# Performance work log

Hardware: AMD Instinct MI355X
Metric: run time of the kernel (lower is better)

Reference implementation:

```python
import jax, jax.numpy as jnp
import numpy as np
import math

B, S, DM = 2, 2048, 2048
NH, NKV, HD = 16, 4, 128
DFF = 8192
K_KEEP = DFF // 2  # sparsity_ratio = 0.5
EPS = 1e-6


def setup_inputs() -> dict:
    key = jax.random.key(0)
    ks = jax.random.split(key, 10)
    sc = 0.02
    return {
        "hidden_states": jax.random.normal(ks[0], (B, S, DM), dtype=jnp.float32),
        "wq": jax.random.normal(ks[1], (NH * HD, DM), dtype=jnp.float32) * sc,
        "wk": jax.random.normal(ks[2], (NKV * HD, DM), dtype=jnp.float32) * sc,
        "wv": jax.random.normal(ks[3], (NKV * HD, DM), dtype=jnp.float32) * sc,
        "wo": jax.random.normal(ks[4], (DM, NH * HD), dtype=jnp.float32) * sc,
        "ln1_w": jnp.ones((DM,), dtype=jnp.float32),
        "ln2_w": jnp.ones((DM,), dtype=jnp.float32),
        "w_gate": jax.random.normal(ks[5], (DFF, DM), dtype=jnp.float32) * sc,
        "w_up": jax.random.normal(ks[6], (DFF, DM), dtype=jnp.float32) * sc,
        "w_down": jax.random.normal(ks[7], (DM, DFF), dtype=jnp.float32) * sc,
    }


def _rmsnorm(x, w):
    var = jnp.mean(x * x, axis=-1, keepdims=True)
    return x * jax.lax.rsqrt(var + EPS) * w


def reference(hidden_states, wq, wk, wv, wo, ln1_w, ln2_w, w_gate, w_up, w_down):
    b, s, _ = hidden_states.shape
    # --- attention sub-block: RMSNorm -> GQA causal attention -> residual ---
    x = _rmsnorm(hidden_states, ln1_w)
    q = (x @ wq.T).reshape(b, s, NH, HD)
    k = (x @ wk.T).reshape(b, s, NKV, HD)
    v = (x @ wv.T).reshape(b, s, NKV, HD)
    # expand KV heads to match query heads (GQA)
    rep = NH // NKV
    k = jnp.repeat(k, rep, axis=2)
    v = jnp.repeat(v, rep, axis=2)
    scores = jnp.einsum('bqhd,bkhd->bhqk', q, k) / math.sqrt(HD)
    causal = jnp.tril(jnp.ones((s, s), dtype=bool))
    scores = jnp.where(causal, scores, jnp.finfo(scores.dtype).min)
    attn = jax.nn.softmax(scores, axis=-1)
    o = jnp.einsum('bhqk,bkhd->bqhd', attn, v).reshape(b, s, NH * HD)
    h = hidden_states + o @ wo.T
    # --- FFN sub-block: RMSNorm -> TopK-sparse SwiGLU -> residual ---
    y = _rmsnorm(h, ln2_w)
    gate = jax.nn.silu(y @ w_gate.T)  # [b, s, DFF]
    mag = jnp.abs(gate)
    thr = jax.lax.top_k(mag, K_KEEP)[0][..., -1:]  # kth-largest magnitude
    gate = jnp.where(mag >= thr, gate, 0.0)
    ff = (gate * (y @ w_up.T)) @ w_down.T
    return h + ff
```

## Files before the change

### kernel.cpp

```cpp
#include <hip/hip_runtime.h>
#include <stdint.h>

constexpr int SEQ    = 2048;
constexpr int DMODEL = 2048;
constexpr int NHEADS = 16;
constexpr int NKVH   = 4;
constexpr int HDIM   = 128;
constexpr int DFFN   = 8192;
constexpr int BATCH  = 2;
constexpr int MTOK   = BATCH * SEQ;
constexpr int KKEEP  = DFFN / 2;

typedef __bf16 bf16x8 __attribute__((ext_vector_type(8)));
typedef float  f32x4  __attribute__((ext_vector_type(4)));
typedef unsigned short u16;
typedef unsigned int   u32;

__device__ __forceinline__ u16 f2bu(float f) {
  u32 x = __builtin_bit_cast(u32, f);
  return (u16)((x + 0x7FFFu + ((x >> 16) & 1u)) >> 16);
}
__device__ __forceinline__ float b2f(u16 u) {
  u32 v = ((u32)u) << 16;
  return __builtin_bit_cast(float, v);
}
__device__ __forceinline__ void gl_lds16(const void* g, void* l) {
  __builtin_amdgcn_global_load_lds((const __attribute__((address_space(1))) u32*)g,
                                   (__attribute__((address_space(3))) u32*)l, 16, 0, 0);
}

__global__ __launch_bounds__(256) void cvt_kernel(const float* __restrict__ in,
                                                  u16* __restrict__ out, int n) {
  int i = (blockIdx.x * 256 + threadIdx.x) * 4;
  if (i >= n) return;
  float4 v = *(const float4*)(in + i);
  uint2 pk;
  pk.x = (u32)f2bu(v.x) | ((u32)f2bu(v.y) << 16);
  pk.y = (u32)f2bu(v.z) | ((u32)f2bu(v.w) << 16);
  *(uint2*)(out + i) = pk;
}

__global__ __launch_bounds__(256) void rmsnorm_kernel(const float* __restrict__ in,
                                                      const float* __restrict__ w,
                                                      u16* __restrict__ out) {
  const int tid = threadIdx.x;
  const size_t row = blockIdx.x;
  const float* x = in + row * DMODEL;
  float4 v0 = *(const float4*)(x + tid * 4);
  float4 v1 = *(const float4*)(x + 1024 + tid * 4);
  float s = v0.x*v0.x + v0.y*v0.y + v0.z*v0.z + v0.w*v0.w
          + v1.x*v1.x + v1.y*v1.y + v1.z*v1.z + v1.w*v1.w;
#pragma unroll
  for (int off = 1; off < 64; off <<= 1) s += __shfl_xor(s, off, 64);
  __shared__ float wsum[4];
  if ((tid & 63) == 0) wsum[tid >> 6] = s;
  __syncthreads();
  s = wsum[0] + wsum[1] + wsum[2] + wsum[3];
  const float rinv = rsqrtf(s * (1.0f / DMODEL) + 1e-6f);
  u16* o = out + row * DMODEL;
#pragma unroll
  for (int part = 0; part < 2; ++part) {
    int c = part * 1024 + tid * 4;
    float4 vv = (part == 0) ? v0 : v1;
    float4 wv = *(const float4*)(w + c);
    uint2 pk;
    pk.x = (u32)f2bu(vv.x * rinv * wv.x) | ((u32)f2bu(vv.y * rinv * wv.y) << 16);
    pk.y = (u32)f2bu(vv.z * rinv * wv.z) | ((u32)f2bu(vv.w * rinv * wv.w) << 16);
    *(uint2*)(o + c) = pk;
  }
}

template <int EPI>
__global__ __launch_bounds__(256, 2)
void gemm_bt(const u16* __restrict__ A, const u16* __restrict__ B,
             void* __restrict__ C, const float* res,
             int M, int N, int K) {
  __shared__ u16 As[128 * 64];
  __shared__ u16 Bs[128 * 64];
  const int tid = threadIdx.x;
  const int wave = tid >> 6, lane = tid & 63;
  const int m0 = blockIdx.y * 128, n0 = blockIdx.x * 128;
  const int r_in = lane >> 3, chk = lane & 7;
  const int fk = lane >> 4, fc = lane & 15;
  const int wm = (wave >> 1) * 64, wn = (wave & 1) * 64;
  f32x4 acc[4][4] = {};

  for (int kt = 0; kt < K; kt += 64) {
    __syncthreads();
#pragma unroll
    for (int i = 0; i < 4; ++i) {
      int row = wave * 32 + i * 8 + r_in;
      int gc = chk ^ (row & 7);
      gl_lds16(A + (size_t)(m0 + row) * K + kt + gc * 8, As + (wave * 32 + i * 8) * 64);
    }
#pragma unroll
    for (int i = 0; i < 4; ++i) {
      int row = wave * 32 + i * 8 + r_in;
      int gc = chk ^ (row & 7);
      gl_lds16(B + (size_t)(n0 + row) * K + kt + gc * 8, Bs + (wave * 32 + i * 8) * 64);
    }
    __syncthreads();
#pragma unroll
    for (int kk = 0; kk < 2; ++kk) {
      bf16x8 a[4], b[4];
#pragma unroll
      for (int i = 0; i < 4; ++i) {
        int row = wm + i * 16 + fc;
        int c = (kk * 4 + fk) ^ (row & 7);
        a[i] = *(const bf16x8*)(As + row * 64 + c * 8);
      }
#pragma unroll
      for (int j = 0; j < 4; ++j) {
        int row = wn + j * 16 + fc;
        int c = (kk * 4 + fk) ^ (row & 7);
        b[j] = *(const bf16x8*)(Bs + row * 64 + c * 8);
      }
#pragma unroll
      for (int i = 0; i < 4; ++i)
#pragma unroll
        for (int j = 0; j < 4; ++j)
          acc[i][j] = __builtin_amdgcn_mfma_f32_16x16x32_bf16(a[i], b[j], acc[i][j], 0, 0, 0);
    }
  }

  const int rb = fk * 4;
#pragma unroll
  for (int i = 0; i < 4; ++i) {
#pragma unroll
    for (int j = 0; j < 4; ++j) {
      int row = m0 + wm + i * 16 + rb;
      int col = n0 + wn + j * 16 + fc;
      f32x4 v = acc[i][j];
      if constexpr (EPI == 0) {
        u16* o = (u16*)C;
#pragma unroll
        for (int r = 0; r < 4; ++r) o[(size_t)(row + r) * N + col] = f2bu(v[r]);
      } else if constexpr (EPI == 1) {
        u16* o = (u16*)C;
        int bb = row >> 11, s = row & (SEQ - 1);
        int kvh = col >> 7, d = col & (HDIM - 1);
        size_t base = (((size_t)bb * NKVH + kvh) * HDIM + d) * SEQ + s;
        uint2 pk;
        pk.x = (u32)f2bu(v[0]) | ((u32)f2bu(v[1]) << 16);
        pk.y = (u32)f2bu(v[2]) | ((u32)f2bu(v[3]) << 16);
        *(uint2*)(o + base) = pk;
      } else if constexpr (EPI == 2) {
        float* o = (float*)C;
#pragma unroll
        for (int r = 0; r < 4; ++r) {
          size_t idx = (size_t)(row + r) * N + col;
          float rv = res[idx];
          o[idx] = v[r] + rv;
        }
      } else {
        float* o = (float*)C;
#pragma unroll
        for (int r = 0; r < 4; ++r) {
          float g = v[r];
          o[(size_t)(row + r) * N + col] = g / (1.0f + __expf(-g));
        }
      }
    }
  }
}

__global__ __launch_bounds__(256, 2)
void attn_kernel(const u16* __restrict__ Q, const u16* __restrict__ Kb,
                 const u16* __restrict__ Vt, u16* __restrict__ O) {
  __shared__ u16 Ks[32 * 128];
  __shared__ u16 Vs[128 * 32];
  __shared__ u16 Ps[4][16 * 32];
  const int tid = threadIdx.x, wave = tid >> 6, lane = tid & 63;
  const int qt = blockIdx.x, h = blockIdx.y, b = blockIdx.z;
  const int kvh = h >> 2;
  const int q0 = qt * 64, qw = q0 + wave * 16;
  const int fk = lane >> 4, fc = lane & 15;
  const float SC = 0.08838834764831845f;

  bf16x8 qf[4];
  {
    const u16* qp = Q + ((size_t)(b * SEQ + qw + fc)) * DMODEL + h * HDIM + fk * 8;
#pragma unroll
    for (int f = 0; f < 4; ++f) qf[f] = *(const bf16x8*)(qp + f * 32);
  }
  f32x4 oacc[8] = {};
  float m_run[4] = {-1e30f, -1e30f, -1e30f, -1e30f};
  float l_run[4] = {0.f, 0.f, 0.f, 0.f};
  const int nt = (q0 + 64) / 32;
  const int kr = lane >> 4, kc = lane & 15;
  const int vr = lane >> 2, vc = lane & 3;

  for (int t = 0; t < nt; ++t) {
    const int k0 = t * 32;
    __syncthreads();
#pragma unroll
    for (int ii = 0; ii < 2; ++ii) {
      int issue = wave * 2 + ii;
      {
        int row = issue * 4 + kr;
        int gc = kc ^ (row & 7);
        gl_lds16(Kb + ((size_t)(b * SEQ + k0 + row)) * (NKVH * HDIM) + kvh * HDIM + gc * 8,
                 Ks + issue * 4 * 128);
      }
      {
        int row = issue * 16 + vr;
        int gc = vc ^ ((row >> 1) & 3);
        gl_lds16(Vt + (((size_t)b * NKVH + kvh) * HDIM + row) * SEQ + k0 + gc * 8,
                 Vs + issue * 16 * 32);
      }
    }
    __syncthreads();
    if (k0 <= qw + 15) {
      f32x4 sf[2] = {};
#pragma unroll
      for (int sb = 0; sb < 2; ++sb) {
#pragma unroll
        for (int f = 0; f < 4; ++f) {
          int kvr = sb * 16 + fc;
          int c = (f * 4 + fk) ^ (kvr & 7);
          bf16x8 kf = *(const bf16x8*)(Ks + kvr * 128 + c * 8);
          sf[sb] = __builtin_amdgcn_mfma_f32_16x16x32_bf16(qf[f], kf, sf[sb], 0, 0, 0);
        }
      }
#pragma unroll
      for (int r = 0; r < 4; ++r) {
        const int qrow = qw + fk * 4 + r;
        float s0 = sf[0][r] * SC, s1 = sf[1][r] * SC;
        if (k0 + fc > qrow) s0 = -1e30f;
        if (k0 + 16 + fc > qrow) s1 = -1e30f;
        float mx = fmaxf(s0, s1);
#pragma unroll
        for (int off = 1; off < 16; off <<= 1) mx = fmaxf(mx, __shfl_xor(mx, off, 64));
        float mnew = fmaxf(m_run[r], mx);
        float p0 = __expf(s0 - mnew), p1 = __expf(s1 - mnew);
        float rs = p0 + p1;
#pragma unroll
        for (int off = 1; off < 16; off <<= 1) rs += __shfl_xor(rs, off, 64);
        float alpha = __expf(m_run[r] - mnew);
        m_run[r] = mnew;
        l_run[r] = l_run[r] * alpha + rs;
#pragma unroll
        for (int f = 0; f < 8; ++f) oacc[f][r] *= alpha;
        const int prow = fk * 4 + r;
        const int key = (prow >> 1) & 3;
        Ps[wave][prow * 32 + ((((fc >> 3)) ^ key) << 3) + (fc & 7)] = f2bu(p0);
        Ps[wave][prow * 32 + ((((fc >> 3) + 2) ^ key) << 3) + (fc & 7)] = f2bu(p1);
      }
      bf16x8 pf = *(const bf16x8*)(&Ps[wave][fc * 32 + ((fk ^ ((fc >> 1) & 3)) << 3)]);
#pragma unroll
      for (int f = 0; f < 8; ++f) {
        int d = f * 16 + fc;
        int c = fk ^ ((d >> 1) & 3);
        bf16x8 vf = *(const bf16x8*)(Vs + d * 32 + c * 8);
        oacc[f] = __builtin_amdgcn_mfma_f32_16x16x32_bf16(pf, vf, oacc[f], 0, 0, 0);
      }
    }
  }
  u16* op = O + ((size_t)(b * SEQ + qw + fk * 4)) * DMODEL + h * HDIM + fc;
#pragma unroll
  for (int r = 0; r < 4; ++r) {
    float inv = 1.0f / l_run[r];
#pragma unroll
    for (int f = 0; f < 8; ++f) op[(size_t)r * DMODEL + f * 16] = f2bu(oacc[f][r] * inv);
  }
}

__global__ __launch_bounds__(256)
void topk_kernel(const float* __restrict__ gate, u16* __restrict__ upact) {
  __shared__ u32 sabs[DFFN];
  __shared__ u32 hist[4][256];
  __shared__ u32 ss[257];
  __shared__ u32 sh_prefix, sh_rem;
  const int tid = threadIdx.x, wave = tid >> 6;
  const size_t row = blockIdx.x;
  const float* g = gate + row * DFFN;
  for (int it = 0; it < 4; ++it) {
    int e = it * 2048 + tid * 8;
    float4 a = *(const float4*)(g + e);
    float4 b = *(const float4*)(g + e + 4);
    sabs[e + 0] = __builtin_bit_cast(u32, a.x);
    sabs[e + 1] = __builtin_bit_cast(u32, a.y);
    sabs[e + 2] = __builtin_bit_cast(u32, a.z);
    sabs[e + 3] = __builtin_bit_cast(u32, a.w);
    sabs[e + 4] = __builtin_bit_cast(u32, b.x);
    sabs[e + 5] = __builtin_bit_cast(u32, b.y);
    sabs[e + 6] = __builtin_bit_cast(u32, b.z);
    sabs[e + 7] = __builtin_bit_cast(u32, b.w);
  }
  if (tid == 0) { sh_prefix = 0; sh_rem = KKEEP; }
  __syncthreads();
  for (int pass = 0; pass < 4; ++pass) {
    const int p = 24 - pass * 8;
    const u32 mask_hi = (pass == 0) ? 0u : (0xFFFFFFFFu << (p + 8));
    for (int i = tid; i < 1024; i += 256) ((u32*)hist)[i] = 0;
    __syncthreads();
    const u32 prefix = sh_prefix, rem = sh_rem;
    for (int it = 0; it < 4; ++it) {
      int e = it * 2048 + tid * 8;
#pragma unroll
      for (int j = 0; j < 8; ++j) {
        u32 mg = sabs[e + j] & 0x7FFFFFFFu;
        if ((mg & mask_hi) == (prefix & mask_hi))
          atomicAdd(&hist[wave][(mg >> p) & 0xFF], 1u);
      }
    }
    __syncthreads();
    ss[tid] = hist[0][tid] + hist[1][tid] + hist[2][tid] + hist[3][tid];
    if (tid == 0) ss[256] = 0;
    __syncthreads();
    for (int off = 1; off < 256; off <<= 1) {
      u32 v = (tid + off < 256) ? ss[tid + off] : 0u;
      __syncthreads();
      ss[tid] += v;
      __syncthreads();
    }
    if (ss[tid] >= rem && ss[tid + 1] < rem) {
      sh_prefix = prefix | ((u32)tid << p);
      sh_rem = rem - ss[tid + 1];
    }
    __syncthreads();
  }
  const u32 thr = sh_prefix;
  u16* ua = upact + row * DFFN;
  for (int it = 0; it < 4; ++it) {
    int e = it * 2048 + tid * 8;
    uint4 uv = *(const uint4*)(ua + e);
    const u16* up16 = (const u16*)&uv;
    u16 outp[8];
#pragma unroll
    for (int j = 0; j < 8; ++j) {
      u32 bits = sabs[e + j];
      u32 mg = bits & 0x7FFFFFFFu;
      float gg = __builtin_bit_cast(float, bits);
      float prod = (mg >= thr) ? gg * b2f(up16[j]) : 0.0f;
      outp[j] = f2bu(prod);
    }
    uint4 ov;
    ov.x = (u32)outp[0] | ((u32)outp[1] << 16);
    ov.y = (u32)outp[2] | ((u32)outp[3] << 16);
    ov.z = (u32)outp[4] | ((u32)outp[5] << 16);
    ov.w = (u32)outp[6] | ((u32)outp[7] << 16);
    *(uint4*)(ua + e) = ov;
  }
}

extern "C" void kernel_launch(void* const* d_in, const int* in_sizes, int n_in,
                              void* d_out, int out_size, void* d_ws, size_t ws_size,
                              hipStream_t stream) {
  const float* hidden = (const float*)d_in[0];
  const float* wq = (const float*)d_in[1];
  const float* wk = (const float*)d_in[2];
  const float* wv = (const float*)d_in[3];
  const float* wo = (const float*)d_in[4];
  const float* ln1 = (const float*)d_in[5];
  const float* ln2 = (const float*)d_in[6];
  const float* wg = (const float*)d_in[7];
  const float* wu = (const float*)d_in[8];
  const float* wd = (const float*)d_in[9];
  float* out = (float*)d_out;
  (void)in_sizes; (void)n_in; (void)out_size;

  size_t off = 0;
  auto alloc = [&](size_t n) { char* r = (char*)d_ws + off; off += (n + 255) & ~(size_t)255; return r; };
  u16* wq_b = (u16*)alloc((size_t)DMODEL * DMODEL * 2);
  u16* wk_b = (u16*)alloc((size_t)NKVH * HDIM * DMODEL * 2);
  u16* wv_b = (u16*)alloc((size_t)NKVH * HDIM * DMODEL * 2);
  u16* wo_b = (u16*)alloc((size_t)DMODEL * DMODEL * 2);
  u16* wg_b = (u16*)alloc((size_t)DFFN * DMODEL * 2);
  u16* tok  = (u16*)alloc((size_t)MTOK * DMODEL * 2);
  u16* upb  = (u16*)alloc((size_t)MTOK * DFFN * 2);
  char* S   = alloc((size_t)(MTOK / 2) * DFFN * 4);
  u16* qb   = (u16*)S;
  u16* kb   = (u16*)(S + (size_t)MTOK * DMODEL * 2);
  u16* vtb  = (u16*)(S + (size_t)MTOK * DMODEL * 2 + (size_t)MTOK * NKVH * HDIM * 2);
  u16* wu_b = (u16*)(S + (size_t)MTOK * DMODEL * 2 + 2 * (size_t)MTOK * NKVH * HDIM * 2);
  float* gateh = (float*)S;
  u16* wd_b = (u16*)S;
  const size_t needed = off;
  if (ws_size < needed) return;

  auto cvt = [&](const float* src, u16* dst, size_t n) {
    cvt_kernel<<<dim3((unsigned)(n / 1024)), 256, 0, stream>>>(src, dst, (int)n);
  };
  cvt(wq, wq_b, (size_t)DMODEL * DMODEL);
  cvt(wk, wk_b, (size_t)NKVH * HDIM * DMODEL);
  cvt(wv, wv_b, (size_t)NKVH * HDIM * DMODEL);
  cvt(wo, wo_b, (size_t)DMODEL * DMODEL);
  cvt(wg, wg_b, (size_t)DFFN * DMODEL);
  cvt(wu, wu_b, (size_t)DFFN * DMODEL);

  rmsnorm_kernel<<<MTOK, 256, 0, stream>>>(hidden, ln1, tok);

  gemm_bt<0><<<dim3(DMODEL / 128, MTOK / 128), 256, 0, stream>>>(
      tok, wq_b, qb, nullptr, MTOK, DMODEL, DMODEL);
  gemm_bt<0><<<dim3(NKVH * HDIM / 128, MTOK / 128), 256, 0, stream>>>(
      tok, wk_b, kb, nullptr, MTOK, NKVH * HDIM, DMODEL);
  gemm_bt<1><<<dim3(NKVH * HDIM / 128, MTOK / 128), 256, 0, stream>>>(
      tok, wv_b, vtb, nullptr, MTOK, NKVH * HDIM, DMODEL);

  attn_kernel<<<dim3(SEQ / 64, NHEADS, BATCH), 256, 0, stream>>>(qb, kb, vtb, tok);

  gemm_bt<2><<<dim3(DMODEL / 128, MTOK / 128), 256, 0, stream>>>(
      tok, wo_b, out, hidden, MTOK, DMODEL, DMODEL);

  rmsnorm_kernel<<<MTOK, 256, 0, stream>>>(out, ln2, tok);

  gemm_bt<0><<<dim3(DFFN / 128, MTOK / 128), 256, 0, stream>>>(
      tok, wu_b, upb, nullptr, MTOK, DFFN, DMODEL);

  for (int half = 0; half < 2; ++half) {
    const u16* yh = tok + (size_t)half * (MTOK / 2) * DMODEL;
    u16* uph = upb + (size_t)half * (MTOK / 2) * DFFN;
    gemm_bt<3><<<dim3(DFFN / 128, (MTOK / 2) / 128), 256, 0, stream>>>(
        yh, wg_b, gateh, nullptr, MTOK / 2, DFFN, DMODEL);
    topk_kernel<<<MTOK / 2, 256, 0, stream>>>(gateh, uph);
  }

  cvt(wd, wd_b, (size_t)DMODEL * DFFN);

  gemm_bt<2><<<dim3(DMODEL / 128, MTOK / 128), 256, 0, stream>>>(
      upb, wd_b, out, out, MTOK, DMODEL, DFFN);
}
```

Baseline: 1.133 ms.

## Rewrite attention with 32x32 MFMA, double-buffered KV, lazy rescale; swizzle GEMM blocks

The attention kernel now uses 128-query blocks with 32 query rows per wave and 32x32x16 MFMAs. It double-buffers the K/V tiles in LDS to overlap loads with compute, and keeps P in registers through lane shuffles instead of staging it in LDS. The softmax skips rescaling unless the running max grows by more than a threshold. The GEMM and attention grids also remap block indices, XCD-style, to improve cache locality. The risks are higher register pressure and fewer attention blocks, which causes more causal load imbalance per block.

```diff
diff --git a/kernel.cpp b/kernel.cpp
--- a/kernel.cpp
+++ b/kernel.cpp
@@ -13,6 +13,7 @@
 
 typedef __bf16 bf16x8 __attribute__((ext_vector_type(8)));
 typedef float  f32x4  __attribute__((ext_vector_type(4)));
+typedef float  f32x16 __attribute__((ext_vector_type(16)));
 typedef unsigned short u16;
 typedef unsigned int   u32;
 
@@ -79,7 +80,10 @@
   __shared__ u16 Bs[128 * 64];
   const int tid = threadIdx.x;
   const int wave = tid >> 6, lane = tid & 63;
-  const int m0 = blockIdx.y * 128, n0 = blockIdx.x * 128;
+  const int nwg = gridDim.x * gridDim.y;
+  const int lin = blockIdx.y * gridDim.x + blockIdx.x;
+  const int swz = (lin & 7) * (nwg >> 3) + (lin >> 3);
+  const int m0 = (swz / gridDim.x) * 128, n0 = (swz % gridDim.x) * 128;
   const int r_in = lane >> 3, chk = lane & 7;
   const int fk = lane >> 4, fc = lane & 15;
   const int wm = (wave >> 1) * 64, wn = (wave & 1) * 64;
@@ -167,101 +171,142 @@
 __global__ __launch_bounds__(256, 2)
 void attn_kernel(const u16* __restrict__ Q, const u16* __restrict__ Kb,
                  const u16* __restrict__ Vt, u16* __restrict__ O) {
-  __shared__ u16 Ks[32 * 128];
-  __shared__ u16 Vs[128 * 32];
-  __shared__ u16 Ps[4][16 * 32];
+  __shared__ u16 Ksh[2 * 32 * 128];
+  __shared__ u16 Vsh[2 * 128 * 32];
   const int tid = threadIdx.x, wave = tid >> 6, lane = tid & 63;
-  const int qt = blockIdx.x, h = blockIdx.y, b = blockIdx.z;
+  const int half = lane >> 5, l31 = lane & 31;
+  const int d_lin = blockIdx.x + gridDim.x * (blockIdx.y + gridDim.y * blockIdx.z);
+  const int lin = (d_lin & 7) * 64 + (d_lin >> 3);
+  const int bx = lin & 15, h = (lin >> 4) & 15, b = lin >> 8;
   const int kvh = h >> 2;
-  const int q0 = qt * 64, qw = q0 + wave * 16;
-  const int fk = lane >> 4, fc = lane & 15;
+  const int qw = bx * 128 + wave * 32;
   const float SC = 0.08838834764831845f;
-
-  bf16x8 qf[4];
+  const int ntb = bx * 4 + 4;
+  const int nmy = bx * 4 + wave;
+
+  bf16x8 qf[8];
   {
-    const u16* qp = Q + ((size_t)(b * SEQ + qw + fc)) * DMODEL + h * HDIM + fk * 8;
-#pragma unroll
-    for (int f = 0; f < 4; ++f) qf[f] = *(const bf16x8*)(qp + f * 32);
-  }
-  f32x4 oacc[8] = {};
-  float m_run[4] = {-1e30f, -1e30f, -1e30f, -1e30f};
-  float l_run[4] = {0.f, 0.f, 0.f, 0.f};
-  const int nt = (q0 + 64) / 32;
-  const int kr = lane >> 4, kc = lane & 15;
-  const int vr = lane >> 2, vc = lane & 3;
-
-  for (int t = 0; t < nt; ++t) {
-    const int k0 = t * 32;
-    __syncthreads();
+    const u16* qp = Q + ((size_t)(b * SEQ + qw + l31)) * DMODEL + h * HDIM + half * 8;
+#pragma unroll
+    for (int s = 0; s < 8; ++s) qf[s] = *(const bf16x8*)(qp + s * 16);
+  }
+  f32x16 oacc[4] = {};
+  float m_run = -1e30f, l_run = 0.0f;
+  const size_t vbase = ((size_t)(b * NKVH + kvh)) * HDIM * SEQ;
+  const u16* kbase = Kb + (size_t)b * SEQ * (NKVH * HDIM) + kvh * HDIM;
+
+  auto stage = [&](int bi, int k0) {
+    u16* Kd = Ksh + bi * 4096;
+    u16* Vd = Vsh + bi * 4096;
 #pragma unroll
     for (int ii = 0; ii < 2; ++ii) {
-      int issue = wave * 2 + ii;
+      int inst = wave * 2 + ii;
       {
-        int row = issue * 4 + kr;
-        int gc = kc ^ (row & 7);
-        gl_lds16(Kb + ((size_t)(b * SEQ + k0 + row)) * (NKVH * HDIM) + kvh * HDIM + gc * 8,
-                 Ks + issue * 4 * 128);
+        int row = inst * 4 + (lane >> 4);
+        int c = (lane & 15) ^ (row & 15);
+        gl_lds16(kbase + (size_t)(k0 + row) * (NKVH * HDIM) + c * 8, Kd + inst * 512);
       }
       {
-        int row = issue * 16 + vr;
-        int gc = vc ^ ((row >> 1) & 3);
-        gl_lds16(Vt + (((size_t)b * NKVH + kvh) * HDIM + row) * SEQ + k0 + gc * 8,
-                 Vs + issue * 16 * 32);
-      }
-    }
-    __syncthreads();
-    if (k0 <= qw + 15) {
-      f32x4 sf[2] = {};
-#pragma unroll
-      for (int sb = 0; sb < 2; ++sb) {
-#pragma unroll
-        for (int f = 0; f < 4; ++f) {
-          int kvr = sb * 16 + fc;
-          int c = (f * 4 + fk) ^ (kvr & 7);
-          bf16x8 kf = *(const bf16x8*)(Ks + kvr * 128 + c * 8);
-          sf[sb] = __builtin_amdgcn_mfma_f32_16x16x32_bf16(qf[f], kf, sf[sb], 0, 0, 0);
+        int row = inst * 16 + (lane >> 2);
+        int c = (lane & 3) ^ ((row >> 1) & 3);
+        gl_lds16(Vt + vbase + (size_t)row * SEQ + k0 + c * 8, Vd + inst * 512);
+      }
+    }
+  };
+
+  stage(0, 0);
+  __syncthreads();
+
+  for (int t = 0; t < ntb; ++t) {
+    if (t + 1 < ntb) stage((t + 1) & 1, (t + 1) * 32);
+    if (t <= nmy) {
+      const u16* Kd = Ksh + (t & 1) * 4096;
+      const u16* Vd = Vsh + (t & 1) * 4096;
+      f32x16 st = {};
+#pragma unroll
+      for (int s = 0; s < 8; ++s) {
+        int c = (half + 2 * s) ^ (l31 & 15);
+        bf16x8 kf = *(const bf16x8*)(Kd + l31 * 128 + c * 8);
+        st = __builtin_amdgcn_mfma_f32_32x32x16_bf16(kf, qf[s], st, 0, 0, 0);
+      }
+      const bool diag = (t * 32 == qw);
+      float sv[16];
+#pragma unroll
+      for (int r = 0; r < 16; ++r) {
+        float x = st[r] * SC;
+        if (diag) {
+          int kvl = (r & 3) + 8 * (r >> 2) + 4 * half;
+          if (kvl > l31) x = -1e30f;
         }
-      }
-#pragma unroll
-      for (int r = 0; r < 4; ++r) {
-        const int qrow = qw + fk * 4 + r;
-        float s0 = sf[0][r] * SC, s1 = sf[1][r] * SC;
-        if (k0 + fc > qrow) s0 = -1e30f;
-        if (k0 + 16 + fc > qrow) s1 = -1e30f;
-        float mx = fmaxf(s0, s1);
-#pragma unroll
-        for (int off = 1; off < 16; off <<= 1) mx = fmaxf(mx, __shfl_xor(mx, off, 64));
-        float mnew = fmaxf(m_run[r], mx);
-        float p0 = __expf(s0 - mnew), p1 = __expf(s1 - mnew);
-        float rs = p0 + p1;
-#pragma unroll
-        for (int off = 1; off < 16; off <<= 1) rs += __shfl_xor(rs, off, 64);
-        float alpha = __expf(m_run[r] - mnew);
-        m_run[r] = mnew;
-        l_run[r] = l_run[r] * alpha + rs;
-#pragma unroll
-        for (int f = 0; f < 8; ++f) oacc[f][r] *= alpha;
-        const int prow = fk * 4 + r;
-        const int key = (prow >> 1) & 3;
-        Ps[wave][prow * 32 + ((((fc >> 3)) ^ key) << 3) + (fc & 7)] = f2bu(p0);
-        Ps[wave][prow * 32 + ((((fc >> 3) + 2) ^ key) << 3) + (fc & 7)] = f2bu(p1);
-      }
-      bf16x8 pf = *(const bf16x8*)(&Ps[wave][fc * 32 + ((fk ^ ((fc >> 1) & 3)) << 3)]);
-#pragma unroll
-      for (int f = 0; f < 8; ++f) {
-        int d = f * 16 + fc;
-        int c = fk ^ ((d >> 1) & 3);
-        bf16x8 vf = *(const bf16x8*)(Vs + d * 32 + c * 8);
-        oacc[f] = __builtin_amdgcn_mfma_f32_16x16x32_bf16(pf, vf, oacc[f], 0, 0, 0);
-      }
-    }
-  }
-  u16* op = O + ((size_t)(b * SEQ + qw + fk * 4)) * DMODEL + h * HDIM + fc;
-#pragma unroll
-  for (int r = 0; r < 4; ++r) {
-    float inv = 1.0f / l_run[r];
-#pragma unroll
-    for (int f = 0; f < 8; ++f) op[(size_t)r * DMODEL + f * 16] = f2bu(oacc[f][r] * inv);
+        sv[r] = x;
+      }
+      float mx = sv[0];
+#pragma unroll
+      for (int r = 1; r < 16; ++r) mx = fmaxf(mx, sv[r]);
+      mx = fmaxf(mx, __shfl_xor(mx, 32, 64));
+      if (__any(mx > m_run + 4.0f)) {
+        float mnew = fmaxf(m_run, mx);
+        float alpha = __expf(m_run - mnew);
+        m_run = mnew;
+        l_run *= alpha;
+#pragma unroll
+        for (int r = 0; r < 16; ++r) {
+          float ar = __shfl(alpha, (r & 3) + 8 * (r >> 2) + 4 * half, 64);
+#pragma unroll
+          for (int dt = 0; dt < 4; ++dt) oacc[dt][r] *= ar;
+        }
+      }
+      float p[16];
+      float rs = 0.0f;
+#pragma unroll
+      for (int r = 0; r < 16; ++r) { p[r] = __expf(sv[r] - m_run); rs += p[r]; }
+      rs += __shfl_xor(rs, 32, 64);
+      l_run += rs;
+      u32 c01 = (u32)f2bu(p[0])  | ((u32)f2bu(p[1])  << 16);
+      u32 c23 = (u32)f2bu(p[2])  | ((u32)f2bu(p[3])  << 16);
+      u32 c45 = (u32)f2bu(p[4])  | ((u32)f2bu(p[5])  << 16);
+      u32 c67 = (u32)f2bu(p[6])  | ((u32)f2bu(p[7])  << 16);
+      u32 c89 = (u32)f2bu(p[8])  | ((u32)f2bu(p[9])  << 16);
+      u32 cAB = (u32)f2bu(p[10]) | ((u32)f2bu(p[11]) << 16);
+      u32 cCD = (u32)f2bu(p[12]) | ((u32)f2bu(p[13]) << 16);
+      u32 cEF = (u32)f2bu(p[14]) | ((u32)f2bu(p[15]) << 16);
+      u32 paw[2][4];
+      {
+        u32 sA = __shfl_xor(c01, 32, 64), sB = __shfl_xor(c23, 32, 64);
+        u32 sC = __shfl_xor(c45, 32, 64), sD = __shfl_xor(c67, 32, 64);
+        paw[0][0] = half ? sC : c01;  paw[0][1] = half ? sD : c23;
+        paw[0][2] = half ? c45 : sA;  paw[0][3] = half ? c67 : sB;
+      }
+      {
+        u32 sA = __shfl_xor(c89, 32, 64), sB = __shfl_xor(cAB, 32, 64);
+        u32 sC = __shfl_xor(cCD, 32, 64), sD = __shfl_xor(cEF, 32, 64);
+        paw[1][0] = half ? sC : c89;  paw[1][1] = half ? sD : cAB;
+        paw[1][2] = half ? cCD : sA;  paw[1][3] = half ? cEF : sB;
+      }
+#pragma unroll
+      for (int ks = 0; ks < 2; ++ks) {
+        bf16x8 paf = __builtin_bit_cast(bf16x8, *(uint4*)&paw[ks][0]);
+#pragma unroll
+        for (int dt = 0; dt < 4; ++dt) {
+          int row = dt * 32 + l31;
+          int c = (half + 2 * ks) ^ ((row >> 1) & 3);
+          bf16x8 vf = *(const bf16x8*)(Vd + row * 32 + c * 8);
+          oacc[dt] = __builtin_amdgcn_mfma_f32_32x32x16_bf16(paf, vf, oacc[dt], 0, 0, 0);
+        }
+      }
+    }
+    __syncthreads();
+  }
+
+  float rinv = 1.0f / l_run;
+  u16* ob = O + ((size_t)(b * SEQ + qw)) * DMODEL + h * HDIM + l31;
+#pragma unroll
+  for (int r = 0; r < 16; ++r) {
+    int qr = (r & 3) + 8 * (r >> 2) + 4 * half;
+    float ir = __shfl(rinv, qr, 64);
+#pragma unroll
+    for (int dt = 0; dt < 4; ++dt)
+      ob[(size_t)qr * DMODEL + dt * 32] = f2bu(oacc[dt][r] * ir);
   }
 }
 
@@ -398,7 +443,7 @@
   gemm_bt<1><<<dim3(NKVH * HDIM / 128, MTOK / 128), 256, 0, stream>>>(
       tok, wv_b, vtb, nullptr, MTOK, NKVH * HDIM, DMODEL);
 
-  attn_kernel<<<dim3(SEQ / 64, NHEADS, BATCH), 256, 0, stream>>>(qb, kb, vtb, tok);
+  attn_kernel<<<dim3(SEQ / 128, NHEADS, BATCH), 256, 0, stream>>>(qb, kb, vtb, tok);
 
   gemm_bt<2><<<dim3(DMODEL / 128, MTOK / 128), 256, 0, stream>>>(
       tok, wo_b, out, hidden, MTOK, DMODEL, DMODEL);
```

Measured after the change: 1.086 ms. -4.2%, faster.
